# Kernel tuning notes

Hardware: AMD Instinct MI355X
Metric: run time of the kernel (lower is better)

The kernel has to match this reference:

```python
import jax, jax.numpy as jnp
import numpy as np

JITTER_NOISE = 0.01


def setup_inputs() -> dict:
    key = jax.random.key(0)
    k1, k2, k3 = jax.random.split(key, 3)
    B, S, H, E = 8, 4096, 2048, 64
    token_inputs = jax.random.normal(k1, (B, S, H), dtype=jnp.float32)
    # multiplicative jitter in [1 - eps, 1 + eps]
    jitter = jax.random.uniform(k2, (B, S, H), dtype=jnp.float32,
                                minval=1.0 - JITTER_NOISE, maxval=1.0 + JITTER_NOISE)
    w = jax.random.normal(k3, (H, E), dtype=jnp.float32) * 0.02
    b = jnp.zeros((E,), dtype=jnp.float32)
    return {"token_inputs": token_inputs, "jitter": jitter, "w": w, "b": b,
            "num_experts": E, "top_k": 2}


def reference(token_inputs, jitter, w, b, num_experts, top_k):
    # float32 routing computation with jitter noise
    x = token_inputs.astype(jnp.float32) * jitter
    # router logits: [B, S, E]
    logits = jnp.einsum('bsh,he->bse', x, w) + b
    probs = jax.nn.softmax(logits, axis=-1)  # [B, S, E]
    # top-k one-hot mask over experts
    top_k_indices = jax.lax.top_k(probs, top_k)[1]          # [B, S, K]
    mask = jax.nn.one_hot(top_k_indices, num_experts,
                          dtype=jnp.float32).sum(axis=-2)    # [B, S, E]
    return probs * mask
```

## Files before the change

kernel.cpp:

```cpp
#include <hip/hip_runtime.h>


#define H   2048
#define E   64
#define NKS 64

typedef __attribute__((ext_vector_type(8))) short bf16x8;
typedef __attribute__((ext_vector_type(4))) float f32x4;

#define GBL(p)  ((const __attribute__((address_space(1))) void*)(p))
#define LDSP(p) ((__attribute__((address_space(3))) void*)(p))

__device__ inline ushort f2bf_rne(float f) {
    union { float f; unsigned u; } c; c.f = f;
    const unsigned r = (c.u + 0x7FFFu + ((c.u >> 16) & 1u)) >> 16;
    return (ushort)r;
}
__device__ inline float bf2f(ushort h) {
    union { unsigned u; float f; } c; c.u = ((unsigned)h) << 16;
    return c.f;
}

__global__ __launch_bounds__(256)
void wpack_kernel(const float* __restrict__ w, ushort* __restrict__ bp)
{
    const int t    = blockIdx.x * 256 + threadIdx.x;
    const int lane = t & 63;
    const int n    = (t >> 6) & 3;
    const int ks   = t >> 8;
    const int c    = lane & 15, g = lane >> 4;

    const float* src = w + (size_t)(ks * 32 + g * 8) * E + n * 16 + c;
    bf16x8 vh, vl;
#pragma unroll
    for (int s = 0; s < 8; ++s) {
        const float  v = src[(size_t)s * E];
        const ushort h = f2bf_rne(v);
        vh[s] = (short)h;
        vl[s] = (short)f2bf_rne(v - bf2f(h));
    }
    ushort* d = bp + ((size_t)(ks * 4 + n) * 2 * 64 + lane) * 8;
    *(bf16x8*)d         = vh;
    *(bf16x8*)(d + 512) = vl;
}

__global__ __launch_bounds__(256, 4)
void router_kernel(const float* __restrict__ xg,
                   const float* __restrict__ jg,
                   const ushort* __restrict__ bp,
                   const float* __restrict__ bias,
                   float* __restrict__ out)
{
    __shared__ __align__(16) unsigned char smem[32768];
    float  (*xs)[32][32] = (float (*)[32][32])(void*)smem;
    float  (*js)[32][32] = (float (*)[32][32])(void*)(smem + 8192);
    ushort (*bs)[512]    = (ushort (*)[512])(void*)(smem + 16384);

    const int tid  = threadIdx.x;
    const int wv   = tid >> 6;
    const int lane = tid & 63;
    const int ln   = lane & 15;
    const int g    = lane >> 4;
    const int mh   = wv >> 1;
    const int nh   = wv & 1;
    const size_t tokBase = (size_t)blockIdx.x * 32;

    const int srow = lane >> 3;
    const int sqd  = ((lane & 7) - srow) & 7;
    const float* xsb = xg + (tokBase + wv * 8 + srow) * (size_t)H + sqd * 4;
    const float* jsb = jg + (tokBase + wv * 8 + srow) * (size_t)H + sqd * 4;
    const ushort* bsb = bp + (size_t)wv * 1024 + (size_t)lane * 8;

    const int t = mh * 16 + ln;

    f32x4 acc0 = (f32x4){0.f, 0.f, 0.f, 0.f};
    f32x4 acc1 = (f32x4){0.f, 0.f, 0.f, 0.f};

#define STAGE(b, c) do {                                                      \
        __builtin_amdgcn_global_load_lds(GBL(xsb + (size_t)(c) * 32),         \
                                         LDSP(&xs[b][wv * 8][0]), 16, 0, 0);  \
        __builtin_amdgcn_global_load_lds(GBL(jsb + (size_t)(c) * 32),         \
                                         LDSP(&js[b][wv * 8][0]), 16, 0, 0);  \
        __builtin_amdgcn_global_load_lds(GBL(bsb + (size_t)(c) * 4096),       \
                                         LDSP(&bs[(b) * 8 + wv * 2][0]), 16, 0, 0); \
        __builtin_amdgcn_global_load_lds(GBL(bsb + (size_t)(c) * 4096 + 512), \
                                         LDSP(&bs[(b) * 8 + wv * 2 + 1][0]), 16, 0, 0); \
    } while (0)

#define COMPUTE(b) do {                                                       \
        const int p0 = ((2 * g + t) & 7) << 2;                                \
        const int p1 = ((2 * g + 1 + t) & 7) << 2;                            \
        const float4 xq0 = *(const float4*)&xs[b][t][p0];                     \
        const float4 xq1 = *(const float4*)&xs[b][t][p1];                     \
        const float4 jq0 = *(const float4*)&js[b][t][p0];                     \
        const float4 jq1 = *(const float4*)&js[b][t][p1];                     \
        float pr[8];                                                          \
        pr[0] = xq0.x * jq0.x; pr[1] = xq0.y * jq0.y;                         \
        pr[2] = xq0.z * jq0.z; pr[3] = xq0.w * jq0.w;                         \
        pr[4] = xq1.x * jq1.x; pr[5] = xq1.y * jq1.y;                         \
        pr[6] = xq1.z * jq1.z; pr[7] = xq1.w * jq1.w;                         \
        bf16x8 ah, al;                                                        \
        _Pragma("unroll")                                                     \
        for (int i_ = 0; i_ < 8; ++i_) {                                      \
            const ushort h_ = f2bf_rne(pr[i_]);                               \
            ah[i_] = (short)h_;                                               \
            al[i_] = (short)f2bf_rne(pr[i_] - bf2f(h_));                      \
        }                                                                     \
        const bf16x8 BH0 = *(const bf16x8*)&bs[(b) * 8 + 4 * nh + 0][lane * 8]; \
        const bf16x8 BL0 = *(const bf16x8*)&bs[(b) * 8 + 4 * nh + 1][lane * 8]; \
        const bf16x8 BH1 = *(const bf16x8*)&bs[(b) * 8 + 4 * nh + 2][lane * 8]; \
        const bf16x8 BL1 = *(const bf16x8*)&bs[(b) * 8 + 4 * nh + 3][lane * 8]; \
        acc0 = __builtin_amdgcn_mfma_f32_16x16x32_bf16(ah, BH0, acc0, 0, 0, 0); \
        acc0 = __builtin_amdgcn_mfma_f32_16x16x32_bf16(al, BH0, acc0, 0, 0, 0); \
        acc0 = __builtin_amdgcn_mfma_f32_16x16x32_bf16(ah, BL0, acc0, 0, 0, 0); \
        acc1 = __builtin_amdgcn_mfma_f32_16x16x32_bf16(ah, BH1, acc1, 0, 0, 0); \
        acc1 = __builtin_amdgcn_mfma_f32_16x16x32_bf16(al, BH1, acc1, 0, 0, 0); \
        acc1 = __builtin_amdgcn_mfma_f32_16x16x32_bf16(ah, BL1, acc1, 0, 0, 0); \
    } while (0)

    STAGE(0, 0);
    __syncthreads();

#pragma unroll 1
    for (int c = 0; c < NKS; c += 2) {
        STAGE(1, c + 1);
        __builtin_amdgcn_sched_barrier(0);
        COMPUTE(0);
        __syncthreads();
        if (c + 2 < NKS) STAGE(0, c + 2);
        __builtin_amdgcn_sched_barrier(0);
        COMPUTE(1);
        __syncthreads();
    }

    float (*lgx)[68] = (float (*)[68])(void*)smem;
#pragma unroll
    for (int r = 0; r < 4; ++r) {
        lgx[mh * 16 + g * 4 + r][nh * 32 + ln]      = acc0[r];
        lgx[mh * 16 + g * 4 + r][nh * 32 + 16 + ln] = acc1[r];
    }
    __syncthreads();

    const int t8 = tid >> 3;
    const int q8 = tid & 7;
    float l[8];
    *(float4*)&l[0] = *(const float4*)&lgx[t8][q8 * 8];
    *(float4*)&l[4] = *(const float4*)&lgx[t8][q8 * 8 + 4];
    const float4 bb0 = *(const float4*)(bias + q8 * 8);
    const float4 bb1 = *(const float4*)(bias + q8 * 8 + 4);
    l[0] += bb0.x; l[1] += bb0.y; l[2] += bb0.z; l[3] += bb0.w;
    l[4] += bb1.x; l[5] += bb1.y; l[6] += bb1.z; l[7] += bb1.w;

    float p1 = l[0]; int i1 = q8 * 8;
    float p2 = -3.0e38f; int i2 = q8 * 8;
#pragma unroll
    for (int i = 1; i < 8; ++i) {
        const int e = q8 * 8 + i;
        if (l[i] > p1)      { p2 = p1; i2 = i1; p1 = l[i]; i1 = e; }
        else if (l[i] > p2) { p2 = l[i]; i2 = e; }
    }

#pragma unroll
    for (int m = 1; m <= 4; m <<= 1) {
        const float q1 = __shfl_xor(p1, m, 8);
        const int   k1 = __shfl_xor(i1, m, 8);
        const float q2 = __shfl_xor(p2, m, 8);
        const int   k2 = __shfl_xor(i2, m, 8);
        const bool  bw = (q1 > p1) || (q1 == p1 && k1 < i1);
        const float f1 = bw ? q1 : p1;  const int fi1 = bw ? k1 : i1;
        const float lo = bw ? p1 : q1;  const int loi = bw ? i1 : k1;
        const float sn = bw ? q2 : p2;  const int sni = bw ? k2 : i2;
        const bool  rw = (lo > sn) || (lo == sn && loi < sni);
        p2 = rw ? lo : sn;  i2 = rw ? loi : sni;
        p1 = f1;            i1 = fi1;
    }

    float d = 0.f;
#pragma unroll
    for (int i = 0; i < 8; ++i) d += __expf(l[i] - p1);
#pragma unroll
    for (int m = 1; m <= 4; m <<= 1) d += __shfl_xor(d, m, 8);

    const float inv = 1.f / d;
    const float w2  = __expf(p2 - p1) * inv;

    float* op = out + (tokBase + t8) * (size_t)E + q8 * 8;
    float4 v0, v1;
    v0.x = (q8 * 8 + 0 == i1) ? inv : (q8 * 8 + 0 == i2) ? w2 : 0.f;
    v0.y = (q8 * 8 + 1 == i1) ? inv : (q8 * 8 + 1 == i2) ? w2 : 0.f;
    v0.z = (q8 * 8 + 2 == i1) ? inv : (q8 * 8 + 2 == i2) ? w2 : 0.f;
    v0.w = (q8 * 8 + 3 == i1) ? inv : (q8 * 8 + 3 == i2) ? w2 : 0.f;
    v1.x = (q8 * 8 + 4 == i1) ? inv : (q8 * 8 + 4 == i2) ? w2 : 0.f;
    v1.y = (q8 * 8 + 5 == i1) ? inv : (q8 * 8 + 5 == i2) ? w2 : 0.f;
    v1.z = (q8 * 8 + 6 == i1) ? inv : (q8 * 8 + 6 == i2) ? w2 : 0.f;
    v1.w = (q8 * 8 + 7 == i1) ? inv : (q8 * 8 + 7 == i2) ? w2 : 0.f;
    *(float4*)op       = v0;
    *(float4*)(op + 4) = v1;
}

extern "C" void kernel_launch(void* const* d_in, const int* in_sizes, int n_in,
                              void* d_out, int out_size, void* d_ws, size_t ws_size,
                              hipStream_t stream)
{
    const float* x   = (const float*)d_in[0];
    const float* jit = (const float*)d_in[1];
    const float* w   = (const float*)d_in[2];
    const float* b   = (const float*)d_in[3];
    float*       out = (float*)d_out;

    ushort* bpack = (ushort*)d_ws;

    hipLaunchKernelGGL(wpack_kernel, dim3(64), dim3(256), 0, stream, w, bpack);

    const int n_tok = in_sizes[0] / H;
    dim3 grid(n_tok / 32), block(256);
    hipLaunchKernelGGL(router_kernel, grid, block, 0, stream,
                       x, jit, bpack, b, out);
}
```

Baseline: 135.5 us.

## Deepen router GEMM pipeline to four LDS stages with vmcnt waits

Replaces the double-buffered LDS pipeline with a four-stage ring buffer, issuing three chunks of loads ahead and waiting with explicit s_waitcnt vmcnt counts instead of full syncthreads drains. LDS use doubles to 64KB and the occupancy hint drops from 4 to 2 blocks per CU. The aim is to keep more global loads in flight per block to hide memory latency in this bandwidth-bound kernel, at the cost of fewer resident blocks.

Result: slower. 161.1 us (+18.9%).

```diff
diff --git a/kernel.cpp b/kernel.cpp
--- a/kernel.cpp
+++ b/kernel.cpp
@@ -44,17 +44,17 @@
     *(bf16x8*)(d + 512) = vl;
 }
 
-__global__ __launch_bounds__(256, 4)
+__global__ __launch_bounds__(256, 2)
 void router_kernel(const float* __restrict__ xg,
                    const float* __restrict__ jg,
                    const ushort* __restrict__ bp,
                    const float* __restrict__ bias,
                    float* __restrict__ out)
 {
-    __shared__ __align__(16) unsigned char smem[32768];
-    float  (*xs)[32][32] = (float (*)[32][32])(void*)smem;
-    float  (*js)[32][32] = (float (*)[32][32])(void*)(smem + 8192);
-    ushort (*bs)[512]    = (ushort (*)[512])(void*)(smem + 16384);
+    __shared__ __align__(16) unsigned char smem[65536];
+#define XS(b) ((float (*)[32])(void*)(smem + (b) * 16384))
+#define JS(b) ((float (*)[32])(void*)(smem + (b) * 16384 + 4096))
+#define BS(b) ((ushort (*)[512])(void*)(smem + (b) * 16384 + 8192))
 
     const int tid  = threadIdx.x;
     const int wv   = tid >> 6;
@@ -76,24 +76,24 @@
     f32x4 acc0 = (f32x4){0.f, 0.f, 0.f, 0.f};
     f32x4 acc1 = (f32x4){0.f, 0.f, 0.f, 0.f};
 
-#define STAGE(b, c) do {                                                      \
+#define STAGE(bb, c) do {                                                     \
         __builtin_amdgcn_global_load_lds(GBL(xsb + (size_t)(c) * 32),         \
-                                         LDSP(&xs[b][wv * 8][0]), 16, 0, 0);  \
+                                         LDSP(&XS(bb)[wv * 8][0]), 16, 0, 0); \
         __builtin_amdgcn_global_load_lds(GBL(jsb + (size_t)(c) * 32),         \
-                                         LDSP(&js[b][wv * 8][0]), 16, 0, 0);  \
+                                         LDSP(&JS(bb)[wv * 8][0]), 16, 0, 0); \
         __builtin_amdgcn_global_load_lds(GBL(bsb + (size_t)(c) * 4096),       \
-                                         LDSP(&bs[(b) * 8 + wv * 2][0]), 16, 0, 0); \
+                                         LDSP(&BS(bb)[wv * 2][0]), 16, 0, 0); \
         __builtin_amdgcn_global_load_lds(GBL(bsb + (size_t)(c) * 4096 + 512), \
-                                         LDSP(&bs[(b) * 8 + wv * 2 + 1][0]), 16, 0, 0); \
-    } while (0)
-
-#define COMPUTE(b) do {                                                       \
+                                         LDSP(&BS(bb)[wv * 2 + 1][0]), 16, 0, 0); \
+    } while (0)
+
+#define COMPUTE(bb) do {                                                      \
         const int p0 = ((2 * g + t) & 7) << 2;                                \
         const int p1 = ((2 * g + 1 + t) & 7) << 2;                            \
-        const float4 xq0 = *(const float4*)&xs[b][t][p0];                     \
-        const float4 xq1 = *(const float4*)&xs[b][t][p1];                     \
-        const float4 jq0 = *(const float4*)&js[b][t][p0];                     \
-        const float4 jq1 = *(const float4*)&js[b][t][p1];                     \
+        const float4 xq0 = *(const float4*)&XS(bb)[t][p0];                    \
+        const float4 xq1 = *(const float4*)&XS(bb)[t][p1];                    \
+        const float4 jq0 = *(const float4*)&JS(bb)[t][p0];                    \
+        const float4 jq1 = *(const float4*)&JS(bb)[t][p1];                    \
         float pr[8];                                                          \
         pr[0] = xq0.x * jq0.x; pr[1] = xq0.y * jq0.y;                         \
         pr[2] = xq0.z * jq0.z; pr[3] = xq0.w * jq0.w;                         \
@@ -106,10 +106,10 @@
             ah[i_] = (short)h_;                                               \
             al[i_] = (short)f2bf_rne(pr[i_] - bf2f(h_));                      \
         }                                                                     \
-        const bf16x8 BH0 = *(const bf16x8*)&bs[(b) * 8 + 4 * nh + 0][lane * 8]; \
-        const bf16x8 BL0 = *(const bf16x8*)&bs[(b) * 8 + 4 * nh + 1][lane * 8]; \
-        const bf16x8 BH1 = *(const bf16x8*)&bs[(b) * 8 + 4 * nh + 2][lane * 8]; \
-        const bf16x8 BL1 = *(const bf16x8*)&bs[(b) * 8 + 4 * nh + 3][lane * 8]; \
+        const bf16x8 BH0 = *(const bf16x8*)&BS(bb)[4 * nh + 0][lane * 8];     \
+        const bf16x8 BL0 = *(const bf16x8*)&BS(bb)[4 * nh + 1][lane * 8];     \
+        const bf16x8 BH1 = *(const bf16x8*)&BS(bb)[4 * nh + 2][lane * 8];     \
+        const bf16x8 BL1 = *(const bf16x8*)&BS(bb)[4 * nh + 3][lane * 8];     \
         acc0 = __builtin_amdgcn_mfma_f32_16x16x32_bf16(ah, BH0, acc0, 0, 0, 0); \
         acc0 = __builtin_amdgcn_mfma_f32_16x16x32_bf16(al, BH0, acc0, 0, 0, 0); \
         acc0 = __builtin_amdgcn_mfma_f32_16x16x32_bf16(ah, BL0, acc0, 0, 0, 0); \
@@ -118,20 +118,38 @@
         acc1 = __builtin_amdgcn_mfma_f32_16x16x32_bf16(ah, BL1, acc1, 0, 0, 0); \
     } while (0)
 
-    STAGE(0, 0);
-    __syncthreads();
+#define VMWAIT(N) do {                                            \
+        asm volatile("s_waitcnt vmcnt(" #N ")" ::: "memory");     \
+        __builtin_amdgcn_sched_barrier(0);                        \
+    } while (0)
+
+#define SBAR() do {                                               \
+        __builtin_amdgcn_sched_barrier(0);                        \
+        __builtin_amdgcn_s_barrier();                             \
+        __builtin_amdgcn_sched_barrier(0);                        \
+    } while (0)
+
+#define SUBSTEP(bb, c) do {                                       \
+        VMWAIT(12); SBAR();                                       \
+        COMPUTE(bb);                                              \
+        SBAR();                                                   \
+        STAGE(bb, (c) + 4);                                       \
+    } while (0)
+
+    STAGE(0, 0); STAGE(1, 1); STAGE(2, 2); STAGE(3, 3);
 
 #pragma unroll 1
-    for (int c = 0; c < NKS; c += 2) {
-        STAGE(1, c + 1);
-        __builtin_amdgcn_sched_barrier(0);
-        COMPUTE(0);
-        __syncthreads();
-        if (c + 2 < NKS) STAGE(0, c + 2);
-        __builtin_amdgcn_sched_barrier(0);
-        COMPUTE(1);
-        __syncthreads();
-    }
+    for (int i = 0; i < 15; ++i) {
+        const int c = i * 4;
+        SUBSTEP(0, c + 0);
+        SUBSTEP(1, c + 1);
+        SUBSTEP(2, c + 2);
+        SUBSTEP(3, c + 3);
+    }
+    VMWAIT(12); SBAR(); COMPUTE(0);
+    VMWAIT(8);  SBAR(); COMPUTE(1);
+    VMWAIT(4);  SBAR(); COMPUTE(2);
+    VMWAIT(0);  SBAR(); COMPUTE(3);
 
     float (*lgx)[68] = (float (*)[68])(void*)smem;
 #pragma unroll
```

## Split K across waves with direct global loads and an LDS reduction

Applied to the files above, without the earlier changes.

Replaces the LDS-staged, double-buffered pipeline (global_load_lds plus barriers every K chunk) with a split-K scheme. Each of the four waves handles a quarter of H for 16 tokens and all 64 experts, reading x, jitter and packed weights straight from global memory into registers. Partial logits are summed through LDS before the unchanged top-2 softmax epilogue. Blocks now cover 16 tokens instead of 32, which doubles the grid and removes the per-chunk syncs, but each wave reads all 64 experts of weights per token tile, so weight traffic per token doubles, and only half the threads run the epilogue.

After: 147.9 us. 9.1% more time.

```diff
diff --git a/kernel.cpp b/kernel.cpp
--- a/kernel.cpp
+++ b/kernel.cpp
@@ -3,13 +3,9 @@
 
 #define H   2048
 #define E   64
-#define NKS 64
 
 typedef __attribute__((ext_vector_type(8))) short bf16x8;
 typedef __attribute__((ext_vector_type(4))) float f32x4;
-
-#define GBL(p)  ((const __attribute__((address_space(1))) void*)(p))
-#define LDSP(p) ((__attribute__((address_space(3))) void*)(p))
 
 __device__ inline ushort f2bf_rne(float f) {
     union { float f; unsigned u; } c; c.f = f;
@@ -51,151 +47,160 @@
                    const float* __restrict__ bias,
                    float* __restrict__ out)
 {
-    __shared__ __align__(16) unsigned char smem[32768];
-    float  (*xs)[32][32] = (float (*)[32][32])(void*)smem;
-    float  (*js)[32][32] = (float (*)[32][32])(void*)(smem + 8192);
-    ushort (*bs)[512]    = (ushort (*)[512])(void*)(smem + 16384);
+    __shared__ float lgx[4][16][68];
 
     const int tid  = threadIdx.x;
     const int wv   = tid >> 6;
     const int lane = tid & 63;
     const int ln   = lane & 15;
     const int g    = lane >> 4;
-    const int mh   = wv >> 1;
-    const int nh   = wv & 1;
-    const size_t tokBase = (size_t)blockIdx.x * 32;
-
-    const int srow = lane >> 3;
-    const int sqd  = ((lane & 7) - srow) & 7;
-    const float* xsb = xg + (tokBase + wv * 8 + srow) * (size_t)H + sqd * 4;
-    const float* jsb = jg + (tokBase + wv * 8 + srow) * (size_t)H + sqd * 4;
-    const ushort* bsb = bp + (size_t)wv * 1024 + (size_t)lane * 8;
-
-    const int t = mh * 16 + ln;
+    const size_t tokBase = (size_t)blockIdx.x * 16;
+
+    const float* xp = xg + (tokBase + ln) * (size_t)H + wv * 512 + g * 8;
+    const float* jp = jg + (tokBase + ln) * (size_t)H + wv * 512 + g * 8;
+    const ushort* bpw = bp + (size_t)(wv * 16) * 4096 + (size_t)lane * 8;
 
     f32x4 acc0 = (f32x4){0.f, 0.f, 0.f, 0.f};
     f32x4 acc1 = (f32x4){0.f, 0.f, 0.f, 0.f};
-
-#define STAGE(b, c) do {                                                      \
-        __builtin_amdgcn_global_load_lds(GBL(xsb + (size_t)(c) * 32),         \
-                                         LDSP(&xs[b][wv * 8][0]), 16, 0, 0);  \
-        __builtin_amdgcn_global_load_lds(GBL(jsb + (size_t)(c) * 32),         \
-                                         LDSP(&js[b][wv * 8][0]), 16, 0, 0);  \
-        __builtin_amdgcn_global_load_lds(GBL(bsb + (size_t)(c) * 4096),       \
-                                         LDSP(&bs[(b) * 8 + wv * 2][0]), 16, 0, 0); \
-        __builtin_amdgcn_global_load_lds(GBL(bsb + (size_t)(c) * 4096 + 512), \
-                                         LDSP(&bs[(b) * 8 + wv * 2 + 1][0]), 16, 0, 0); \
-    } while (0)
-
-#define COMPUTE(b) do {                                                       \
-        const int p0 = ((2 * g + t) & 7) << 2;                                \
-        const int p1 = ((2 * g + 1 + t) & 7) << 2;                            \
-        const float4 xq0 = *(const float4*)&xs[b][t][p0];                     \
-        const float4 xq1 = *(const float4*)&xs[b][t][p1];                     \
-        const float4 jq0 = *(const float4*)&js[b][t][p0];                     \
-        const float4 jq1 = *(const float4*)&js[b][t][p1];                     \
-        float pr[8];                                                          \
-        pr[0] = xq0.x * jq0.x; pr[1] = xq0.y * jq0.y;                         \
-        pr[2] = xq0.z * jq0.z; pr[3] = xq0.w * jq0.w;                         \
-        pr[4] = xq1.x * jq1.x; pr[5] = xq1.y * jq1.y;                         \
-        pr[6] = xq1.z * jq1.z; pr[7] = xq1.w * jq1.w;                         \
-        bf16x8 ah, al;                                                        \
-        _Pragma("unroll")                                                     \
-        for (int i_ = 0; i_ < 8; ++i_) {                                      \
-            const ushort h_ = f2bf_rne(pr[i_]);                               \
-            ah[i_] = (short)h_;                                               \
-            al[i_] = (short)f2bf_rne(pr[i_] - bf2f(h_));                      \
-        }                                                                     \
-        const bf16x8 BH0 = *(const bf16x8*)&bs[(b) * 8 + 4 * nh + 0][lane * 8]; \
-        const bf16x8 BL0 = *(const bf16x8*)&bs[(b) * 8 + 4 * nh + 1][lane * 8]; \
-        const bf16x8 BH1 = *(const bf16x8*)&bs[(b) * 8 + 4 * nh + 2][lane * 8]; \
-        const bf16x8 BL1 = *(const bf16x8*)&bs[(b) * 8 + 4 * nh + 3][lane * 8]; \
-        acc0 = __builtin_amdgcn_mfma_f32_16x16x32_bf16(ah, BH0, acc0, 0, 0, 0); \
-        acc0 = __builtin_amdgcn_mfma_f32_16x16x32_bf16(al, BH0, acc0, 0, 0, 0); \
-        acc0 = __builtin_amdgcn_mfma_f32_16x16x32_bf16(ah, BL0, acc0, 0, 0, 0); \
-        acc1 = __builtin_amdgcn_mfma_f32_16x16x32_bf16(ah, BH1, acc1, 0, 0, 0); \
-        acc1 = __builtin_amdgcn_mfma_f32_16x16x32_bf16(al, BH1, acc1, 0, 0, 0); \
-        acc1 = __builtin_amdgcn_mfma_f32_16x16x32_bf16(ah, BL1, acc1, 0, 0, 0); \
-    } while (0)
-
-    STAGE(0, 0);
+    f32x4 acc2 = (f32x4){0.f, 0.f, 0.f, 0.f};
+    f32x4 acc3 = (f32x4){0.f, 0.f, 0.f, 0.f};
+
+#pragma unroll 2
+    for (int ks = 0; ks < 16; ++ks) {
+        const float* xq = xp + ks * 32;
+        const float* jq = jp + ks * 32;
+        const float4 x0 = *(const float4*)(xq);
+        const float4 x1 = *(const float4*)(xq + 4);
+        const float4 j0 = *(const float4*)(jq);
+        const float4 j1 = *(const float4*)(jq + 4);
+
+        float pr[8];
+        pr[0] = x0.x * j0.x; pr[1] = x0.y * j0.y;
+        pr[2] = x0.z * j0.z; pr[3] = x0.w * j0.w;
+        pr[4] = x1.x * j1.x; pr[5] = x1.y * j1.y;
+        pr[6] = x1.z * j1.z; pr[7] = x1.w * j1.w;
+
+        bf16x8 ah, al;
+#pragma unroll
+        for (int i = 0; i < 8; ++i) {
+            const ushort h = f2bf_rne(pr[i]);
+            ah[i] = (short)h;
+            al[i] = (short)f2bf_rne(pr[i] - bf2f(h));
+        }
+
+        const ushort* bq = bpw + (size_t)ks * 4096;
+        {
+            const bf16x8 BH = *(const bf16x8*)(bq);
+            const bf16x8 BL = *(const bf16x8*)(bq + 512);
+            acc0 = __builtin_amdgcn_mfma_f32_16x16x32_bf16(ah, BH, acc0, 0, 0, 0);
+            acc0 = __builtin_amdgcn_mfma_f32_16x16x32_bf16(al, BH, acc0, 0, 0, 0);
+            acc0 = __builtin_amdgcn_mfma_f32_16x16x32_bf16(ah, BL, acc0, 0, 0, 0);
+        }
+        {
+            const bf16x8 BH = *(const bf16x8*)(bq + 1024);
+            const bf16x8 BL = *(const bf16x8*)(bq + 1536);
+            acc1 = __builtin_amdgcn_mfma_f32_16x16x32_bf16(ah, BH, acc1, 0, 0, 0);
+            acc1 = __builtin_amdgcn_mfma_f32_16x16x32_bf16(al, BH, acc1, 0, 0, 0);
+            acc1 = __builtin_amdgcn_mfma_f32_16x16x32_bf16(ah, BL, acc1, 0, 0, 0);
+        }
+        {
+            const bf16x8 BH = *(const bf16x8*)(bq + 2048);
+            const bf16x8 BL = *(const bf16x8*)(bq + 2560);
+            acc2 = __builtin_amdgcn_mfma_f32_16x16x32_bf16(ah, BH, acc2, 0, 0, 0);
+            acc2 = __builtin_amdgcn_mfma_f32_16x16x32_bf16(al, BH, acc2, 0, 0, 0);
+            acc2 = __builtin_amdgcn_mfma_f32_16x16x32_bf16(ah, BL, acc2, 0, 0, 0);
+        }
+        {
+            const bf16x8 BH = *(const bf16x8*)(bq + 3072);
+            const bf16x8 BL = *(const bf16x8*)(bq + 3584);
+            acc3 = __builtin_amdgcn_mfma_f32_16x16x32_bf16(ah, BH, acc3, 0, 0, 0);
+            acc3 = __builtin_amdgcn_mfma_f32_16x16x32_bf16(al, BH, acc3, 0, 0, 0);
+            acc3 = __builtin_amdgcn_mfma_f32_16x16x32_bf16(ah, BL, acc3, 0, 0, 0);
+        }
+    }
+
+#pragma unroll
+    for (int r = 0; r < 4; ++r) {
+        lgx[wv][g * 4 + r][     ln] = acc0[r];
+        lgx[wv][g * 4 + r][16 + ln] = acc1[r];
+        lgx[wv][g * 4 + r][32 + ln] = acc2[r];
+        lgx[wv][g * 4 + r][48 + ln] = acc3[r];
+    }
     __syncthreads();
 
-#pragma unroll 1
-    for (int c = 0; c < NKS; c += 2) {
-        STAGE(1, c + 1);
-        __builtin_amdgcn_sched_barrier(0);
-        COMPUTE(0);
-        __syncthreads();
-        if (c + 2 < NKS) STAGE(0, c + 2);
-        __builtin_amdgcn_sched_barrier(0);
-        COMPUTE(1);
-        __syncthreads();
-    }
-
-    float (*lgx)[68] = (float (*)[68])(void*)smem;
-#pragma unroll
-    for (int r = 0; r < 4; ++r) {
-        lgx[mh * 16 + g * 4 + r][nh * 32 + ln]      = acc0[r];
-        lgx[mh * 16 + g * 4 + r][nh * 32 + 16 + ln] = acc1[r];
-    }
-    __syncthreads();
-
-    const int t8 = tid >> 3;
-    const int q8 = tid & 7;
-    float l[8];
-    *(float4*)&l[0] = *(const float4*)&lgx[t8][q8 * 8];
-    *(float4*)&l[4] = *(const float4*)&lgx[t8][q8 * 8 + 4];
-    const float4 bb0 = *(const float4*)(bias + q8 * 8);
-    const float4 bb1 = *(const float4*)(bias + q8 * 8 + 4);
-    l[0] += bb0.x; l[1] += bb0.y; l[2] += bb0.z; l[3] += bb0.w;
-    l[4] += bb1.x; l[5] += bb1.y; l[6] += bb1.z; l[7] += bb1.w;
-
-    float p1 = l[0]; int i1 = q8 * 8;
-    float p2 = -3.0e38f; int i2 = q8 * 8;
-#pragma unroll
-    for (int i = 1; i < 8; ++i) {
-        const int e = q8 * 8 + i;
-        if (l[i] > p1)      { p2 = p1; i2 = i1; p1 = l[i]; i1 = e; }
-        else if (l[i] > p2) { p2 = l[i]; i2 = e; }
-    }
-
-#pragma unroll
-    for (int m = 1; m <= 4; m <<= 1) {
-        const float q1 = __shfl_xor(p1, m, 8);
-        const int   k1 = __shfl_xor(i1, m, 8);
-        const float q2 = __shfl_xor(p2, m, 8);
-        const int   k2 = __shfl_xor(i2, m, 8);
-        const bool  bw = (q1 > p1) || (q1 == p1 && k1 < i1);
-        const float f1 = bw ? q1 : p1;  const int fi1 = bw ? k1 : i1;
-        const float lo = bw ? p1 : q1;  const int loi = bw ? i1 : k1;
-        const float sn = bw ? q2 : p2;  const int sni = bw ? k2 : i2;
-        const bool  rw = (lo > sn) || (lo == sn && loi < sni);
-        p2 = rw ? lo : sn;  i2 = rw ? loi : sni;
-        p1 = f1;            i1 = fi1;
-    }
-
-    float d = 0.f;
-#pragma unroll
-    for (int i = 0; i < 8; ++i) d += __expf(l[i] - p1);
-#pragma unroll
-    for (int m = 1; m <= 4; m <<= 1) d += __shfl_xor(d, m, 8);
-
-    const float inv = 1.f / d;
-    const float w2  = __expf(p2 - p1) * inv;
-
-    float* op = out + (tokBase + t8) * (size_t)E + q8 * 8;
-    float4 v0, v1;
-    v0.x = (q8 * 8 + 0 == i1) ? inv : (q8 * 8 + 0 == i2) ? w2 : 0.f;
-    v0.y = (q8 * 8 + 1 == i1) ? inv : (q8 * 8 + 1 == i2) ? w2 : 0.f;
-    v0.z = (q8 * 8 + 2 == i1) ? inv : (q8 * 8 + 2 == i2) ? w2 : 0.f;
-    v0.w = (q8 * 8 + 3 == i1) ? inv : (q8 * 8 + 3 == i2) ? w2 : 0.f;
-    v1.x = (q8 * 8 + 4 == i1) ? inv : (q8 * 8 + 4 == i2) ? w2 : 0.f;
-    v1.y = (q8 * 8 + 5 == i1) ? inv : (q8 * 8 + 5 == i2) ? w2 : 0.f;
-    v1.z = (q8 * 8 + 6 == i1) ? inv : (q8 * 8 + 6 == i2) ? w2 : 0.f;
-    v1.w = (q8 * 8 + 7 == i1) ? inv : (q8 * 8 + 7 == i2) ? w2 : 0.f;
-    *(float4*)op       = v0;
-    *(float4*)(op + 4) = v1;
+    if (tid < 128) {
+        const int t8 = tid >> 3;
+        const int q8 = tid & 7;
+        const int eb = q8 * 8;
+
+        float l[8];
+        {
+            const float4 a0 = *(const float4*)&lgx[0][t8][eb];
+            const float4 a1 = *(const float4*)&lgx[1][t8][eb];
+            const float4 a2 = *(const float4*)&lgx[2][t8][eb];
+            const float4 a3 = *(const float4*)&lgx[3][t8][eb];
+            const float4 b0 = *(const float4*)&lgx[0][t8][eb + 4];
+            const float4 b1 = *(const float4*)&lgx[1][t8][eb + 4];
+            const float4 b2 = *(const float4*)&lgx[2][t8][eb + 4];
+            const float4 b3 = *(const float4*)&lgx[3][t8][eb + 4];
+            const float4 bb0 = *(const float4*)(bias + eb);
+            const float4 bb1 = *(const float4*)(bias + eb + 4);
+            l[0] = a0.x + a1.x + a2.x + a3.x + bb0.x;
+            l[1] = a0.y + a1.y + a2.y + a3.y + bb0.y;
+            l[2] = a0.z + a1.z + a2.z + a3.z + bb0.z;
+            l[3] = a0.w + a1.w + a2.w + a3.w + bb0.w;
+            l[4] = b0.x + b1.x + b2.x + b3.x + bb1.x;
+            l[5] = b0.y + b1.y + b2.y + b3.y + bb1.y;
+            l[6] = b0.z + b1.z + b2.z + b3.z + bb1.z;
+            l[7] = b0.w + b1.w + b2.w + b3.w + bb1.w;
+        }
+
+        float p1 = l[0]; int i1 = eb;
+        float p2 = -3.0e38f; int i2 = eb;
+#pragma unroll
+        for (int i = 1; i < 8; ++i) {
+            const int e = eb + i;
+            if (l[i] > p1)      { p2 = p1; i2 = i1; p1 = l[i]; i1 = e; }
+            else if (l[i] > p2) { p2 = l[i]; i2 = e; }
+        }
+
+#pragma unroll
+        for (int m = 1; m <= 4; m <<= 1) {
+            const float q1 = __shfl_xor(p1, m, 8);
+            const int   k1 = __shfl_xor(i1, m, 8);
+            const float q2 = __shfl_xor(p2, m, 8);
+            const int   k2 = __shfl_xor(i2, m, 8);
+            const bool  bw = (q1 > p1) || (q1 == p1 && k1 < i1);
+            const float f1 = bw ? q1 : p1;  const int fi1 = bw ? k1 : i1;
+            const float lo = bw ? p1 : q1;  const int loi = bw ? i1 : k1;
+            const float sn = bw ? q2 : p2;  const int sni = bw ? k2 : i2;
+            const bool  rw = (lo > sn) || (lo == sn && loi < sni);
+            p2 = rw ? lo : sn;  i2 = rw ? loi : sni;
+            p1 = f1;            i1 = fi1;
+        }
+
+        float d = 0.f;
+#pragma unroll
+        for (int i = 0; i < 8; ++i) d += __expf(l[i] - p1);
+#pragma unroll
+        for (int m = 1; m <= 4; m <<= 1) d += __shfl_xor(d, m, 8);
+
+        const float inv = 1.f / d;
+        const float w2  = __expf(p2 - p1) * inv;
+
+        float* op = out + (tokBase + t8) * (size_t)E + eb;
+        float4 v0, v1;
+        v0.x = (eb + 0 == i1) ? inv : (eb + 0 == i2) ? w2 : 0.f;
+        v0.y = (eb + 1 == i1) ? inv : (eb + 1 == i2) ? w2 : 0.f;
+        v0.z = (eb + 2 == i1) ? inv : (eb + 2 == i2) ? w2 : 0.f;
+        v0.w = (eb + 3 == i1) ? inv : (eb + 3 == i2) ? w2 : 0.f;
+        v1.x = (eb + 4 == i1) ? inv : (eb + 4 == i2) ? w2 : 0.f;
+        v1.y = (eb + 5 == i1) ? inv : (eb + 5 == i2) ? w2 : 0.f;
+        v1.z = (eb + 6 == i1) ? inv : (eb + 6 == i2) ? w2 : 0.f;
+        v1.w = (eb + 7 == i1) ? inv : (eb + 7 == i2) ? w2 : 0.f;
+        *(float4*)op       = v0;
+        *(float4*)(op + 4) = v1;
+    }
 }
 
 extern "C" void kernel_launch(void* const* d_in, const int* in_sizes, int n_in,
@@ -213,7 +218,7 @@
     hipLaunchKernelGGL(wpack_kernel, dim3(64), dim3(256), 0, stream, w, bpack);
 
     const int n_tok = in_sizes[0] / H;
-    dim3 grid(n_tok / 32), block(256);
+    dim3 grid(n_tok / 16), block(256);
     hipLaunchKernelGGL(router_kernel, grid, block, 0, stream,
                        x, jit, bpack, b, out);
 }
```
